# Kernel tuning notes

Measured on AMD Instinct MI355X. Metric: run time of the kernel, lower is better.

Reference implementation:

```python
import jax, jax.numpy as jnp
import numpy as np

N, E, F_, D, L, G, H, O = 50000, 1600000, 64, 16, 3, 64, 256, 2
EPS = 1e-5


def setup_inputs() -> dict:
    key = jax.random.key(0)
    ks = jax.random.split(key, 16)
    x = jax.random.normal(ks[0], (N, F_), jnp.float32)
    edge_index = jax.random.randint(ks[1], (2, E), 0, N, jnp.int32)
    edge_attr = jax.random.normal(ks[2], (E, D), jnp.float32)
    batch = jnp.sort(jax.random.randint(ks[3], (N,), 0, G, jnp.int32))
    Zin = 2 * F_ + D
    s = 1.0 / np.sqrt(Zin)
    Wf = jax.random.uniform(ks[4], (L, Zin, F_), jnp.float32, -s, s)
    bf = jax.random.uniform(ks[5], (L, F_), jnp.float32, -s, s)
    Ws = jax.random.uniform(ks[6], (L, Zin, F_), jnp.float32, -s, s)
    bs = jax.random.uniform(ks[7], (L, F_), jnp.float32, -s, s)
    bn_g = jnp.ones((L, F_), jnp.float32)
    bn_b = jnp.zeros((L, F_), jnp.float32)
    bn_m = 0.1 * jax.random.normal(ks[8], (L, F_), jnp.float32)
    bn_v = jnp.ones((L, F_), jnp.float32) + 0.1 * jax.random.uniform(ks[9], (L, F_), jnp.float32)
    s1 = 1.0 / np.sqrt(F_)
    W1 = jax.random.uniform(ks[10], (F_, H), jnp.float32, -s1, s1)
    b1 = jax.random.uniform(ks[11], (H,), jnp.float32, -s1, s1)
    bn2_g = jnp.ones((H,), jnp.float32)
    bn2_b = jnp.zeros((H,), jnp.float32)
    bn2_m = 0.1 * jax.random.normal(ks[12], (H,), jnp.float32)
    bn2_v = jnp.ones((H,), jnp.float32) + 0.1 * jax.random.uniform(ks[13], (H,), jnp.float32)
    s2 = 1.0 / np.sqrt(H)
    W2 = jax.random.uniform(ks[14], (H, O), jnp.float32, -s2, s2)
    b2 = jax.random.uniform(ks[15], (O,), jnp.float32, -s2, s2)
    return {"x": x, "edge_index": edge_index, "edge_attr": edge_attr, "batch": batch,
            "Wf": Wf, "bf": bf, "Ws": Ws, "bs": bs,
            "bn_g": bn_g, "bn_b": bn_b, "bn_m": bn_m, "bn_v": bn_v,
            "W1": W1, "b1": b1, "bn2_g": bn2_g, "bn2_b": bn2_b,
            "bn2_m": bn2_m, "bn2_v": bn2_v, "W2": W2, "b2": b2}


def reference(x, edge_index, edge_attr, batch, Wf, bf, Ws, bs, bn_g, bn_b, bn_m, bn_v,
              W1, b1, bn2_g, bn2_b, bn2_m, bn2_v, W2, b2):
    src, dst = edge_index[0], edge_index[1]  # PyG: x_j = x[src], x_i = x[dst]
    for l in range(L):
        # gather per-edge features: [E, 2F+D]
        z = jnp.concatenate([x[dst], x[src], edge_attr], axis=-1)
        # CGConv message: sigmoid gate (lin_f) * softplus (lin_s)
        msg = jax.nn.sigmoid(z @ Wf[l] + bf[l]) * jax.nn.softplus(z @ Ws[l] + bs[l])
        agg = jax.ops.segment_sum(msg, dst, num_segments=N)  # scatter-add to targets
        # BatchNorm1d (inference: running stats), then residual
        agg = (agg - bn_m[l]) * jax.lax.rsqrt(bn_v[l] + EPS) * bn_g[l] + bn_b[l]
        x = x + agg
    pooled = jax.ops.segment_max(x, batch, num_segments=G)  # global max pool per graph
    h = jax.nn.relu(pooled @ W1 + b1)
    h = (h - bn2_m) * jax.lax.rsqrt(bn2_v + EPS) * bn2_g + bn2_b
    return jax.nn.sigmoid(h @ W2 + b2)
```

## Files before the change

kernel.cpp:

```cpp
#include <hip/hip_runtime.h>
#include <math.h>

constexpr int N_  = 50000;
constexpr int E_  = 1600000;
constexpr int F   = 64;
constexpr int DEA = 16;
constexpr int LL  = 3;
constexpr int GG  = 64;
constexpr int HH  = 256;
constexpr int OO  = 2;
constexpr int ZIN = 2 * F + DEA;
#define EPS_ 1e-5f

typedef float v2f __attribute__((ext_vector_type(2)));

#define LOG2E_ 1.44269504f
#define LN2_ 0.69314718f

__device__ __forceinline__ unsigned int fmap(float f) {
  unsigned int u = __float_as_uint(f);
  return (u & 0x80000000u) ? ~u : (u | 0x80000000u);
}
__device__ __forceinline__ float funmap(unsigned int m) {
  return (m & 0x80000000u) ? __uint_as_float(m ^ 0x80000000u)
                           : __uint_as_float(~m);
}
__device__ __forceinline__ unsigned f2bf(float f) {
  unsigned u = __float_as_uint(f);
  return (u + 0x7FFFu + ((u >> 16) & 1u)) >> 16;
}

__global__ __launch_bounds__(256) void node_linear_k(
    const float* __restrict__ x, const float* __restrict__ Wf,
    const float* __restrict__ bf, const float* __restrict__ Ws,
    const float* __restrict__ bs, float2* __restrict__ Darr,
    unsigned* __restrict__ SarrP) {
  __shared__ float xs[4][64];
  const int wave = threadIdx.x >> 6, lane = threadIdx.x & 63;
  const int n = blockIdx.x * 4 + wave;
  xs[wave][lane] = x[n * 64 + lane];
  __syncthreads();
  float df = 0.f, ds = 0.f, sf = 0.f, ss = 0.f;
#pragma unroll 8
  for (int d = 0; d < 64; ++d) {
    const float xv = xs[wave][d];
    df += xv * Wf[d * 64 + lane];
    sf += xv * Wf[(64 + d) * 64 + lane];
    ds += xv * Ws[d * 64 + lane];
    ss += xv * Ws[(64 + d) * 64 + lane];
  }
  Darr[n * 64 + lane] = make_float2(df + bf[lane], ds + bs[lane]);
  SarrP[n * 64 + lane] = f2bf(sf) | (f2bf(ss) << 16);
}

__global__ __launch_bounds__(256) void hist_k(const int* __restrict__ dst,
                                              int* __restrict__ cnt) {
  const int e = blockIdx.x * 256 + threadIdx.x;
  atomicAdd(&cnt[dst[e]], 1);
}

constexpr int SCAN_T = 1024;
constexpr int CHUNK = 52;

__global__ __launch_bounds__(SCAN_T) void scan_k(const int* __restrict__ cnt,
                                                 int* __restrict__ rowptr,
                                                 int* __restrict__ cursor) {
  __shared__ int s[SCAN_T];
  const int t = threadIdx.x;
  int vals[CHUNK];
  const int base = t * CHUNK;
#pragma unroll
  for (int j = 0; j < CHUNK / 4; ++j) {
    const int4 v = *(const int4*)(cnt + base + j * 4);
    vals[j * 4 + 0] = v.x;
    vals[j * 4 + 1] = v.y;
    vals[j * 4 + 2] = v.z;
    vals[j * 4 + 3] = v.w;
  }
  int partial = 0;
#pragma unroll
  for (int j = 0; j < CHUNK; ++j)
    if (base + j < N_) partial += vals[j];
  s[t] = partial;
  __syncthreads();
  for (int off = 1; off < SCAN_T; off <<= 1) {
    int v = (t >= off) ? s[t - off] : 0;
    __syncthreads();
    s[t] += v;
    __syncthreads();
  }
  int run = s[t] - partial;
#pragma unroll
  for (int j = 0; j < CHUNK; ++j) {
    const int idx = base + j;
    if (idx < N_) {
      rowptr[idx] = run;
      cursor[idx] = run;
      run += vals[j];
    } else if (idx == N_) {
      rowptr[idx] = run;
    }
  }
}

__global__ __launch_bounds__(256) void scatter_k(
    const int* __restrict__ src, const int* __restrict__ dst,
    const float* __restrict__ ea, int* __restrict__ cursor,
    int* __restrict__ csr_src, float* __restrict__ ea_csr) {
  const int e = blockIdx.x * 256 + threadIdx.x;
  const int d = dst[e];
  const int pos = atomicAdd(&cursor[d], 1);
  csr_src[pos] = src[e];
  const float4* s4 = (const float4*)(ea + (size_t)e * DEA);
  float4* d4 = (float4*)(ea_csr + (size_t)pos * DEA);
  d4[0] = s4[0];
  d4[1] = s4[1];
  d4[2] = s4[2];
  d4[3] = s4[3];
}

__global__ __launch_bounds__(256) void edge_agg_k(
    const int* __restrict__ rowptr, const int* __restrict__ csr_src,
    const float* __restrict__ ea_csr, const float* __restrict__ WfE,
    const float* __restrict__ WsE, const float2* __restrict__ Darr,
    const unsigned* __restrict__ SarrP, const float* __restrict__ xin,
    const float* __restrict__ g, const float* __restrict__ b,
    const float* __restrict__ m, const float* __restrict__ v,
    float* __restrict__ xout, int nwaves_total) {
  const int lane = threadIdx.x & 63;
  const int wid = blockIdx.x * 4 + (threadIdx.x >> 6);
  v2f w[DEA];
#pragma unroll
  for (int d = 0; d < DEA; ++d) {
    w[d].x = WfE[d * 64 + lane];
    w[d].y = WsE[d * 64 + lane];
  }
#pragma unroll
  for (int d = 0; d < DEA; ++d) asm volatile("" : "+v"(w[d]));
  const float bnm = m[lane];
  const float bnsc = rsqrtf(v[lane] + EPS_) * g[lane];
  const float bnb = b[lane];
  for (int n = wid; n < N_; n += nwaves_total) {
    const int nu = __builtin_amdgcn_readfirstlane(n);
    const int r0 = rowptr[nu], r1 = rowptr[nu + 1];
    const float2 dvl = Darr[nu * 64 + lane];
    const v2f dv = {dvl.x, dvl.y};
    float acc = 0.f;
    if (r0 < r1) {
      unsigned p_cur = SarrP[(size_t)csr_src[r0] * 64 + lane];
      for (int i = r0; i < r1; ++i) {
        const int iu = __builtin_amdgcn_readfirstlane(i);
        const int inx = (iu + 1 < r1) ? iu + 1 : iu;
        const unsigned p_next = SarrP[(size_t)csr_src[inx] * 64 + lane];
        const float* eap = ea_csr + (size_t)iu * DEA;
        v2f gv = dv;
        gv.x += __uint_as_float(p_cur << 16);
        gv.y += __uint_as_float(p_cur & 0xFFFF0000u);
#pragma unroll
        for (int d = 0; d < DEA; ++d) gv += eap[d] * w[d];
        const float sig = __builtin_amdgcn_rcpf(
            1.f + __builtin_amdgcn_exp2f(gv.x * -LOG2E_));
        const float t = __builtin_amdgcn_exp2f(-fabsf(gv.y) * LOG2E_);
        const float sp =
            fmaxf(gv.y, 0.f) + LN2_ * __builtin_amdgcn_logf(1.f + t);
        acc = fmaf(sig, sp, acc);
        p_cur = p_next;
      }
    }
    xout[nu * 64 + lane] = xin[nu * 64 + lane] + (acc - bnm) * bnsc + bnb;
  }
}

__global__ __launch_bounds__(256) void pool_max_k(
    const float* __restrict__ x, const int* __restrict__ batch,
    unsigned int* __restrict__ pooled) {
  const int wave_glob = blockIdx.x * 4 + (threadIdx.x >> 6);
  const int lane = threadIdx.x & 63;
  const int n0 = wave_glob * 32;
  if (n0 >= N_) return;
  const int nend = min(n0 + 32, N_);
  int cur_b = batch[n0];
  float mmax = -INFINITY;
  for (int n = n0; n < nend; ++n) {
    const int b = batch[n];
    if (b != cur_b) {
      atomicMax(&pooled[cur_b * 64 + lane], fmap(mmax));
      cur_b = b;
      mmax = -INFINITY;
    }
    mmax = fmaxf(mmax, x[n * 64 + lane]);
  }
  atomicMax(&pooled[cur_b * 64 + lane], fmap(mmax));
}

__global__ __launch_bounds__(256) void head1_k(
    const unsigned int* __restrict__ pooled, const float* __restrict__ W1,
    const float* __restrict__ b1, const float* __restrict__ g2,
    const float* __restrict__ b2n, const float* __restrict__ m2,
    const float* __restrict__ v2, float* __restrict__ h) {
  __shared__ float p[64];
  const int gidx = blockIdx.x;
  const int j = threadIdx.x;
  if (j < 64) p[j] = funmap(pooled[gidx * 64 + j]);
  __syncthreads();
  float acc = b1[j];
#pragma unroll 8
  for (int k = 0; k < 64; ++k) acc += p[k] * W1[k * HH + j];
  acc = fmaxf(acc, 0.f);
  acc = (acc - m2[j]) * rsqrtf(v2[j] + EPS_) * g2[j] + b2n[j];
  h[gidx * HH + j] = acc;
}

__global__ __launch_bounds__(128) void head2_k(
    const float* __restrict__ h, const float* __restrict__ W2,
    const float* __restrict__ b2, float* __restrict__ out) {
  const int t = threadIdx.x;
  const int gidx = t >> 1, o = t & 1;
  float acc = b2[o];
#pragma unroll 8
  for (int k = 0; k < HH; ++k) acc += h[gidx * HH + k] * W2[k * OO + o];
  out[gidx * OO + o] = 1.f / (1.f + __expf(-acc));
}

extern "C" void kernel_launch(void* const* d_in, const int* in_sizes, int n_in,
                              void* d_out, int out_size, void* d_ws,
                              size_t ws_size, hipStream_t stream) {
  const float* x    = (const float*)d_in[0];
  const int* ei     = (const int*)d_in[1];
  const float* ea   = (const float*)d_in[2];
  const int* batch  = (const int*)d_in[3];
  const float* Wf   = (const float*)d_in[4];
  const float* bf   = (const float*)d_in[5];
  const float* Ws   = (const float*)d_in[6];
  const float* bs   = (const float*)d_in[7];
  const float* bn_g = (const float*)d_in[8];
  const float* bn_b = (const float*)d_in[9];
  const float* bn_m = (const float*)d_in[10];
  const float* bn_v = (const float*)d_in[11];
  const float* W1   = (const float*)d_in[12];
  const float* b1   = (const float*)d_in[13];
  const float* g2   = (const float*)d_in[14];
  const float* b2n  = (const float*)d_in[15];
  const float* m2   = (const float*)d_in[16];
  const float* v2   = (const float*)d_in[17];
  const float* W2   = (const float*)d_in[18];
  const float* b2   = (const float*)d_in[19];
  float* out = (float*)d_out;

  char* ws = (char*)d_ws;
  float2* Darr   = (float2*)ws;
  unsigned* SarrP = (unsigned*)(Darr + (size_t)N_ * 64);
  float* x_cur   = (float*)(SarrP + (size_t)N_ * 64);
  int* cnt       = (int*)(x_cur + (size_t)N_ * F);
  int* rowptr    = cnt + N_;
  int* cursor    = rowptr + (N_ + 4);
  int* csr_src   = cursor + (N_ + 4);
  float* ea_csr  = (float*)(csr_src + E_);
  unsigned int* pooled = (unsigned int*)(ea_csr + (size_t)E_ * DEA);
  float* h_ws    = (float*)(pooled + GG * F);

  const int* srcp = ei;
  const int* dstp = ei + E_;

  constexpr int EDGE_BLOCKS = 2048;
  constexpr int EDGE_WAVES = EDGE_BLOCKS * 4;

  hipMemsetAsync(cnt, 0, N_ * sizeof(int), stream);
  hist_k<<<E_ / 256, 256, 0, stream>>>(dstp, cnt);
  scan_k<<<1, SCAN_T, 0, stream>>>(cnt, rowptr, cursor);
  scatter_k<<<E_ / 256, 256, 0, stream>>>(srcp, dstp, ea, cursor, csr_src,
                                          ea_csr);

  for (int l = 0; l < LL; ++l) {
    const float* xin = (l == 0) ? x : x_cur;
    node_linear_k<<<N_ / 4, 256, 0, stream>>>(
        xin, Wf + (size_t)l * ZIN * F, bf + l * F, Ws + (size_t)l * ZIN * F,
        bs + l * F, Darr, SarrP);
    edge_agg_k<<<EDGE_BLOCKS, 256, 0, stream>>>(
        rowptr, csr_src, ea_csr, Wf + (size_t)l * ZIN * F + 2 * F * F,
        Ws + (size_t)l * ZIN * F + 2 * F * F, Darr, SarrP, xin,
        bn_g + l * F, bn_b + l * F, bn_m + l * F, bn_v + l * F, x_cur,
        EDGE_WAVES);
  }
  hipMemsetAsync(pooled, 0, GG * F * sizeof(unsigned int), stream);
  const int nwaves = (N_ + 31) / 32;
  pool_max_k<<<(nwaves + 3) / 4, 256, 0, stream>>>(x_cur, batch, pooled);
  head1_k<<<GG, 256, 0, stream>>>(pooled, W1, b1, g2, b2n, m2, v2, h_ws);
  head2_k<<<1, 128, 0, stream>>>(h_ws, W2, b2, out);
}
```

Baseline: 1.218 ms.

## Register-block node linear, deepen edge gather prefetch, fuse max-pool into last layer

```diff
diff --git a/kernel.cpp b/kernel.cpp
--- a/kernel.cpp
+++ b/kernel.cpp
@@ -35,22 +35,36 @@
     const float* __restrict__ bf, const float* __restrict__ Ws,
     const float* __restrict__ bs, float2* __restrict__ Darr,
     unsigned* __restrict__ SarrP) {
-  __shared__ float xs[4][64];
+  __shared__ float xs[16][64];
   const int wave = threadIdx.x >> 6, lane = threadIdx.x & 63;
-  const int n = blockIdx.x * 4 + wave;
-  xs[wave][lane] = x[n * 64 + lane];
-  __syncthreads();
-  float df = 0.f, ds = 0.f, sf = 0.f, ss = 0.f;
-#pragma unroll 8
+  const int nb = blockIdx.x * 16;
+#pragma unroll
+  for (int j = 0; j < 4; ++j)
+    xs[wave * 4 + j][lane] = x[(nb + wave * 4 + j) * 64 + lane];
+  float df[4] = {0, 0, 0, 0}, sf[4] = {0, 0, 0, 0};
+  float ds[4] = {0, 0, 0, 0}, ss[4] = {0, 0, 0, 0};
+#pragma unroll 4
   for (int d = 0; d < 64; ++d) {
-    const float xv = xs[wave][d];
-    df += xv * Wf[d * 64 + lane];
-    sf += xv * Wf[(64 + d) * 64 + lane];
-    ds += xv * Ws[d * 64 + lane];
-    ss += xv * Ws[(64 + d) * 64 + lane];
-  }
-  Darr[n * 64 + lane] = make_float2(df + bf[lane], ds + bs[lane]);
-  SarrP[n * 64 + lane] = f2bf(sf) | (f2bf(ss) << 16);
+    const float wf0 = Wf[d * 64 + lane];
+    const float wf1 = Wf[(64 + d) * 64 + lane];
+    const float ws0 = Ws[d * 64 + lane];
+    const float ws1 = Ws[(64 + d) * 64 + lane];
+#pragma unroll
+    for (int j = 0; j < 4; ++j) {
+      const float xv = xs[wave * 4 + j][d];
+      df[j] = fmaf(xv, wf0, df[j]);
+      sf[j] = fmaf(xv, wf1, sf[j]);
+      ds[j] = fmaf(xv, ws0, ds[j]);
+      ss[j] = fmaf(xv, ws1, ss[j]);
+    }
+  }
+  const float bfl = bf[lane], bsl = bs[lane];
+#pragma unroll
+  for (int j = 0; j < 4; ++j) {
+    const int n = nb + wave * 4 + j;
+    Darr[n * 64 + lane] = make_float2(df[j] + bfl, ds[j] + bsl);
+    SarrP[n * 64 + lane] = f2bf(sf[j]) | (f2bf(ss[j]) << 16);
+  }
 }
 
 __global__ __launch_bounds__(256) void hist_k(const int* __restrict__ dst,
@@ -119,6 +133,7 @@
   d4[3] = s4[3];
 }
 
+template <bool LAST>
 __global__ __launch_bounds__(256) void edge_agg_k(
     const int* __restrict__ rowptr, const int* __restrict__ csr_src,
     const float* __restrict__ ea_csr, const float* __restrict__ WfE,
@@ -126,7 +141,8 @@
     const unsigned* __restrict__ SarrP, const float* __restrict__ xin,
     const float* __restrict__ g, const float* __restrict__ b,
     const float* __restrict__ m, const float* __restrict__ v,
-    float* __restrict__ xout, int nwaves_total) {
+    float* __restrict__ xout, const int* __restrict__ batch,
+    unsigned* __restrict__ pooled, int nwaves_total) {
   const int lane = threadIdx.x & 63;
   const int wid = blockIdx.x * 4 + (threadIdx.x >> 6);
   v2f w[DEA];
@@ -147,15 +163,18 @@
     const v2f dv = {dvl.x, dvl.y};
     float acc = 0.f;
     if (r0 < r1) {
-      unsigned p_cur = SarrP[(size_t)csr_src[r0] * 64 + lane];
+      const int last = r1 - 1;
+      unsigned p0 = SarrP[(size_t)csr_src[r0] * 64 + lane];
+      const int i1 = (r0 + 1 <= last) ? r0 + 1 : last;
+      unsigned p1 = SarrP[(size_t)csr_src[i1] * 64 + lane];
       for (int i = r0; i < r1; ++i) {
         const int iu = __builtin_amdgcn_readfirstlane(i);
-        const int inx = (iu + 1 < r1) ? iu + 1 : iu;
-        const unsigned p_next = SarrP[(size_t)csr_src[inx] * 64 + lane];
+        const int i2 = (iu + 2 <= last) ? iu + 2 : last;
+        const unsigned p2 = SarrP[(size_t)csr_src[i2] * 64 + lane];
         const float* eap = ea_csr + (size_t)iu * DEA;
         v2f gv = dv;
-        gv.x += __uint_as_float(p_cur << 16);
-        gv.y += __uint_as_float(p_cur & 0xFFFF0000u);
+        gv.x += __uint_as_float(p0 << 16);
+        gv.y += __uint_as_float(p0 & 0xFFFF0000u);
 #pragma unroll
         for (int d = 0; d < DEA; ++d) gv += eap[d] * w[d];
         const float sig = __builtin_amdgcn_rcpf(
@@ -164,33 +183,18 @@
         const float sp =
             fmaxf(gv.y, 0.f) + LN2_ * __builtin_amdgcn_logf(1.f + t);
         acc = fmaf(sig, sp, acc);
-        p_cur = p_next;
+        p0 = p1;
+        p1 = p2;
       }
     }
-    xout[nu * 64 + lane] = xin[nu * 64 + lane] + (acc - bnm) * bnsc + bnb;
-  }
-}
-
-__global__ __launch_bounds__(256) void pool_max_k(
-    const float* __restrict__ x, const int* __restrict__ batch,
-    unsigned int* __restrict__ pooled) {
-  const int wave_glob = blockIdx.x * 4 + (threadIdx.x >> 6);
-  const int lane = threadIdx.x & 63;
-  const int n0 = wave_glob * 32;
-  if (n0 >= N_) return;
-  const int nend = min(n0 + 32, N_);
-  int cur_b = batch[n0];
-  float mmax = -INFINITY;
-  for (int n = n0; n < nend; ++n) {
-    const int b = batch[n];
-    if (b != cur_b) {
-      atomicMax(&pooled[cur_b * 64 + lane], fmap(mmax));
-      cur_b = b;
-      mmax = -INFINITY;
-    }
-    mmax = fmaxf(mmax, x[n * 64 + lane]);
-  }
-  atomicMax(&pooled[cur_b * 64 + lane], fmap(mmax));
+    const float xv = xin[nu * 64 + lane] + (acc - bnm) * bnsc + bnb;
+    if constexpr (LAST) {
+      const int bidx = batch[nu];
+      atomicMax(&pooled[bidx * 64 + lane], fmap(xv));
+    } else {
+      xout[nu * 64 + lane] = xv;
+    }
+  }
 }
 
 __global__ __launch_bounds__(256) void head1_k(
@@ -266,6 +270,7 @@
   constexpr int EDGE_WAVES = EDGE_BLOCKS * 4;
 
   hipMemsetAsync(cnt, 0, N_ * sizeof(int), stream);
+  hipMemsetAsync(pooled, 0, GG * F * sizeof(unsigned int), stream);
   hist_k<<<E_ / 256, 256, 0, stream>>>(dstp, cnt);
   scan_k<<<1, SCAN_T, 0, stream>>>(cnt, rowptr, cursor);
   scatter_k<<<E_ / 256, 256, 0, stream>>>(srcp, dstp, ea, cursor, csr_src,
@@ -273,18 +278,23 @@
 
   for (int l = 0; l < LL; ++l) {
     const float* xin = (l == 0) ? x : x_cur;
-    node_linear_k<<<N_ / 4, 256, 0, stream>>>(
+    node_linear_k<<<N_ / 16, 256, 0, stream>>>(
         xin, Wf + (size_t)l * ZIN * F, bf + l * F, Ws + (size_t)l * ZIN * F,
         bs + l * F, Darr, SarrP);
-    edge_agg_k<<<EDGE_BLOCKS, 256, 0, stream>>>(
-        rowptr, csr_src, ea_csr, Wf + (size_t)l * ZIN * F + 2 * F * F,
-        Ws + (size_t)l * ZIN * F + 2 * F * F, Darr, SarrP, xin,
-        bn_g + l * F, bn_b + l * F, bn_m + l * F, bn_v + l * F, x_cur,
-        EDGE_WAVES);
-  }
-  hipMemsetAsync(pooled, 0, GG * F * sizeof(unsigned int), stream);
-  const int nwaves = (N_ + 31) / 32;
-  pool_max_k<<<(nwaves + 3) / 4, 256, 0, stream>>>(x_cur, batch, pooled);
+    const float* WfEl = Wf + (size_t)l * ZIN * F + 2 * F * F;
+    const float* WsEl = Ws + (size_t)l * ZIN * F + 2 * F * F;
+    if (l < LL - 1) {
+      edge_agg_k<false><<<EDGE_BLOCKS, 256, 0, stream>>>(
+          rowptr, csr_src, ea_csr, WfEl, WsEl, Darr, SarrP, xin,
+          bn_g + l * F, bn_b + l * F, bn_m + l * F, bn_v + l * F, x_cur,
+          batch, pooled, EDGE_WAVES);
+    } else {
+      edge_agg_k<true><<<EDGE_BLOCKS, 256, 0, stream>>>(
+          rowptr, csr_src, ea_csr, WfEl, WsEl, Darr, SarrP, xin,
+          bn_g + l * F, bn_b + l * F, bn_m + l * F, bn_v + l * F, x_cur,
+          batch, pooled, EDGE_WAVES);
+    }
+  }
   head1_k<<<GG, 256, 0, stream>>>(pooled, W1, b1, g2, b2n, m2, v2, h_ws);
   head2_k<<<1, 128, 0, stream>>>(h_ws, W2, b2, out);
 }
```

New measurement: 1.044 ms. 14.2% less time.
